# Kernel tuning notes

Hardware: AMD Instinct MI355X
Metric: run time of the kernel (lower is better)

## Reference

```python
import jax, jax.numpy as jnp
import numpy as np

B, T, D, H, L, V = 4, 1024, 1024, 16, 6, 32000
HS = D // H
FF = 4 * D
EPS = 1e-5


def setup_inputs() -> dict:
    key = jax.random.key(0)
    ks = jax.random.split(key, 16)
    s = 0.02
    n = lambda k, shape: (jax.random.normal(k, shape, jnp.float32) * s)
    return {
        'idx': jax.random.randint(ks[0], (B, T), 0, V),
        'targets': jax.random.randint(ks[1], (B, T), 0, V),
        'tok_emb': n(ks[2], (V, D)),
        'pos_emb': n(ks[3], (T, D)),
        'Wq': n(ks[4], (L, D, H, HS)),
        'Wk': n(ks[5], (L, D, H, HS)),
        'Wv': n(ks[6], (L, D, H, HS)),
        'proj_w': n(ks[7], (L, D, D)),
        'proj_b': jnp.zeros((L, D), jnp.float32),
        'ln1_g': jnp.ones((L, D), jnp.float32),
        'ln1_b': jnp.zeros((L, D), jnp.float32),
        'ln2_g': jnp.ones((L, D), jnp.float32),
        'ln2_b': jnp.zeros((L, D), jnp.float32),
        'ff_w1': n(ks[8], (L, D, FF)),
        'ff_b1': jnp.zeros((L, FF), jnp.float32),
        'ff_w2': n(ks[9], (L, FF, D)),
        'ff_b2': jnp.zeros((L, D), jnp.float32),
        'lnf_g': jnp.ones((D,), jnp.float32),
        'lnf_b': jnp.zeros((D,), jnp.float32),
        'head_w': n(ks[10], (D, V)),
        'head_b': jnp.zeros((V,), jnp.float32),
    }


def _ln(x, g, b):
    m = jnp.mean(x, axis=-1, keepdims=True)
    v = jnp.mean((x - m) ** 2, axis=-1, keepdims=True)
    return (x - m) * jax.lax.rsqrt(v + EPS) * g + b


def _forward(idx, targets, tok_emb, pos_emb, Wq, Wk, Wv, proj_w, proj_b,
             ln1_g, ln1_b, ln2_g, ln2_b, ff_w1, ff_b1, ff_w2, ff_b2,
             lnf_g, lnf_b, head_w, head_b):
    b, t = idx.shape
    x = tok_emb[idx] + pos_emb[:t]                       # [B,T,D]
    mask = jnp.tril(jnp.ones((t, t), bool))              # causal
    scale = jnp.float32(D) ** -0.5                       # NOTE: scales by num_dims (c), as in source
    for l in range(L):
        h = _ln(x, ln1_g[l], ln1_b[l])
        q = jnp.einsum('btd,dhs->bhts', h, Wq[l])        # [B,H,T,HS]
        k = jnp.einsum('btd,dhs->bhts', h, Wk[l])
        v = jnp.einsum('btd,dhs->bhts', h, Wv[l])
        w = jnp.einsum('bhts,bhus->bhtu', q, k) * scale  # [B,H,T,T]
        w = jnp.where(mask, w, -jnp.inf)
        w = jax.nn.softmax(w, axis=-1)
        o = jnp.einsum('bhtu,bhus->bhts', w, v)          # [B,H,T,HS]
        o = o.transpose(0, 2, 1, 3).reshape(b, t, D)     # concat heads
        x = x + jnp.einsum('btd,de->bte', o, proj_w[l]) + proj_b[l]
        h2 = _ln(x, ln2_g[l], ln2_b[l])
        ff = jax.nn.relu(jnp.einsum('btd,df->btf', h2, ff_w1[l]) + ff_b1[l])
        x = x + jnp.einsum('btf,fd->btd', ff, ff_w2[l]) + ff_b2[l]
    x = _ln(x, lnf_g, lnf_b)
    logits = jnp.einsum('btd,dv->btv', x, head_w) + head_b
    logits = logits.reshape(b * t, V)
    tgt = targets.reshape(b * t)
    logp = jax.nn.log_softmax(logits, axis=-1)
    loss = -jnp.mean(jnp.take_along_axis(logp, tgt[:, None], axis=-1))
    return logits, loss


def reference(idx, targets, tok_emb, pos_emb, Wq, Wk, Wv, proj_w, proj_b,
              ln1_g, ln1_b, ln2_g, ln2_b, ff_w1, ff_b1, ff_w2, ff_b2,
              lnf_g, lnf_b, head_w, head_b):
    return _forward(idx, targets, tok_emb, pos_emb, Wq, Wk, Wv, proj_w, proj_b,
                    ln1_g, ln1_b, ln2_g, ln2_b, ff_w1, ff_b1, ff_w2, ff_b2,
                    lnf_g, lnf_b, head_w, head_b)
```

## Files before the change

### kernel.cpp

```cpp
#include <hip/hip_runtime.h>

typedef __attribute__((ext_vector_type(8))) short bf16x8;
typedef __attribute__((ext_vector_type(4))) float f32x4;

#define L_LAYERS 6
#define T_SEQ 1024
#define D_MODEL 1024
#define N_HEAD 16
#define HS 64
#define FF_DIM 4096
#define VOCAB 32000
#define BT_ROWS 4096
#define ATTN_SCALE 0.03125f

__device__ __forceinline__ ushort f2bf(float f) {
  unsigned u = __builtin_bit_cast(unsigned, f);
  unsigned r = (u + 0x7fffu + ((u >> 16) & 1u)) >> 16;
  return (ushort)r;
}
__device__ __forceinline__ float waveRedSum(float v) {
#pragma unroll
  for (int off = 32; off; off >>= 1) v += __shfl_xor(v, off);
  return v;
}
__device__ __forceinline__ void gload16(const void* g, void* l) {
  __builtin_amdgcn_global_load_lds(
      (const __attribute__((address_space(1))) unsigned int*)g,
      (__attribute__((address_space(3))) unsigned int*)l, 16, 0, 0);
}

__global__ __launch_bounds__(256) void embed_kernel(const int* __restrict__ idx,
                                                    const float* __restrict__ tok,
                                                    const float* __restrict__ pos,
                                                    float* __restrict__ x) {
  int row = blockIdx.x;
  int tid = threadIdx.x;
  int t = row & (T_SEQ - 1);
  int id = idx[row];
  float4 tv = ((const float4*)(tok + (size_t)id * D_MODEL))[tid];
  float4 pv = ((const float4*)(pos + (size_t)t * D_MODEL))[tid];
  tv.x += pv.x; tv.y += pv.y; tv.z += pv.z; tv.w += pv.w;
  ((float4*)(x + (size_t)row * D_MODEL))[tid] = tv;
}

__global__ __launch_bounds__(256) void ln_kernel(const float* __restrict__ x,
                                                 const float* __restrict__ g,
                                                 const float* __restrict__ b,
                                                 ushort* __restrict__ out) {
  int row = blockIdx.x;
  int tid = threadIdx.x;
  __shared__ float red[4];
  float4 xv = ((const float4*)(x + (size_t)row * D_MODEL))[tid];
  float s = xv.x + xv.y + xv.z + xv.w;
  s = waveRedSum(s);
  if ((tid & 63) == 0) red[tid >> 6] = s;
  __syncthreads();
  float mean = (red[0] + red[1] + red[2] + red[3]) * (1.0f / D_MODEL);
  __syncthreads();
  float d0 = xv.x - mean, d1 = xv.y - mean, d2 = xv.z - mean, d3 = xv.w - mean;
  float v = d0 * d0 + d1 * d1 + d2 * d2 + d3 * d3;
  v = waveRedSum(v);
  if ((tid & 63) == 0) red[tid >> 6] = v;
  __syncthreads();
  float var = (red[0] + red[1] + red[2] + red[3]) * (1.0f / D_MODEL);
  float rstd = rsqrtf(var + 1e-5f);
  float4 gv = ((const float4*)g)[tid];
  float4 bv = ((const float4*)b)[tid];
  ushort4 o;
  o.x = f2bf(d0 * rstd * gv.x + bv.x);
  o.y = f2bf(d1 * rstd * gv.y + bv.y);
  o.z = f2bf(d2 * rstd * gv.z + bv.z);
  o.w = f2bf(d3 * rstd * gv.w + bv.w);
  ((ushort4*)(out + (size_t)row * D_MODEL))[tid] = o;
}

__device__ __forceinline__ void wconv_body(const float* __restrict__ W,
                                           ushort* __restrict__ WT,
                                           int Kd, int Nd, int n0, int k0) {
  __shared__ ushort tile[64][72];
  int tid = threadIdx.x;
#pragma unroll
  for (int i = 0; i < 4; i++) {
    int c = tid + i * 256;
    int row = c >> 4, cc = c & 15;
    float4 wv = *(const float4*)&W[(size_t)(k0 + row) * Nd + n0 + cc * 4];
    tile[row][cc * 4 + 0] = f2bf(wv.x);
    tile[row][cc * 4 + 1] = f2bf(wv.y);
    tile[row][cc * 4 + 2] = f2bf(wv.z);
    tile[row][cc * 4 + 3] = f2bf(wv.w);
  }
  __syncthreads();
#pragma unroll
  for (int i = 0; i < 2; i++) {
    int c = tid + i * 256;
    int n = c >> 3, kc = c & 7;
    __align__(16) ushort tmp[8];
#pragma unroll
    for (int j = 0; j < 8; j++) tmp[j] = tile[kc * 8 + j][n];
    *(int4*)&WT[(size_t)(n0 + n) * Kd + k0 + kc * 8] = *(const int4*)tmp;
  }
}

__global__ __launch_bounds__(256) void wconv_kernel(const float* __restrict__ W,
                                                    ushort* __restrict__ WT,
                                                    int Kd, int Nd) {
  wconv_body(W, WT, Kd, Nd, blockIdx.x * 64, blockIdx.y * 64);
}

__global__ __launch_bounds__(256) void wconv4_kernel(const float* __restrict__ W0,
                                                     const float* __restrict__ W1,
                                                     const float* __restrict__ W2,
                                                     const float* __restrict__ W3,
                                                     ushort* __restrict__ WT,
                                                     int Kd, int Nd) {
  int z = blockIdx.z;
  const float* W = (z == 0) ? W0 : (z == 1) ? W1 : (z == 2) ? W2 : W3;
  wconv_body(W, WT + (size_t)z * Kd * Nd, Kd, Nd, blockIdx.x * 64, blockIdx.y * 64);
}

__global__ __launch_bounds__(256) void vtrans_kernel(const ushort* __restrict__ v,
                                                     ushort* __restrict__ vT) {
  __shared__ ushort tile[64][72];
  int bh = blockIdx.y;
  int t0 = blockIdx.x * 64;
  int tid = threadIdx.x;
#pragma unroll
  for (int i = 0; i < 2; i++) {
    int c = tid + i * 256;
    int row = c >> 3, cc = c & 7;
    *(int4*)&tile[row][cc * 8] =
        *(const int4*)&v[((size_t)bh * T_SEQ + t0 + row) * HS + cc * 8];
  }
  __syncthreads();
#pragma unroll
  for (int i = 0; i < 2; i++) {
    int c = tid + i * 256;
    int hs = c >> 3, tc = c & 7;
    __align__(16) ushort tmp[8];
#pragma unroll
    for (int j = 0; j < 8; j++) tmp[j] = tile[tc * 8 + j][hs];
    *(int4*)&vT[((size_t)bh * HS + hs) * T_SEQ + t0 + tc * 8] = *(const int4*)tmp;
  }
}

template <int BM, int BN, int WM, int WN, int EPI>
__global__ __launch_bounds__(WM * WN * 64, 2) void gemmp_kernel(
    const ushort* __restrict__ A, const ushort* __restrict__ BT, int K,
    const float* __restrict__ bias, float* __restrict__ outf,
    ushort* __restrict__ outb, ushort* __restrict__ outk,
    ushort* __restrict__ outv, int ldo) {
  constexpr int PM = BM / WM, PN = BN / WN;
  constexpr int MR = PM / 16, NR = PN / 16;
  constexpr int ROWS = BM + BN;
  constexpr int NWAVES = WM * WN;
  constexpr int LPW = (ROWS / 8) / NWAVES;
  __shared__ __align__(16) ushort buf[2][ROWS * 64];
  int tid = threadIdx.x;
  int lane = tid & 63, wave = tid >> 6;
  int wm = wave / WN, wn = wave % WN;
  int a = lane & 15, gg = lane >> 4;
  int srow8 = lane >> 3;
  int scol8 = ((lane & 7) ^ (lane >> 3)) * 8;
  int m0 = blockIdx.y * BM, n0 = blockIdx.x * BN;
  f32x4 acc[MR][NR] = {};
  int nt = K >> 6;

  auto STAGE = [&](int t, int d) {
    int k0 = t * 64;
#pragma unroll
    for (int j = 0; j < LPW; j++) {
      int r0 = (wave * LPW + j) * 8;
      if (r0 < BM) {
        gload16(&A[(size_t)(m0 + r0 + srow8) * K + k0 + scol8], &buf[d][r0 * 64]);
      } else {
        gload16(&BT[(size_t)(n0 + (r0 - BM) + srow8) * K + k0 + scol8], &buf[d][r0 * 64]);
      }
    }
  };

  auto COMPUTE = [&](int d) {
    const ushort* bA = &buf[d][0];
    const ushort* bB = &buf[d][BM * 64];
#pragma unroll
    for (int s = 0; s < 2; s++) {
      bf16x8 af[MR], bfr[NR];
#pragma unroll
      for (int i = 0; i < MR; i++) {
        int row = wm * PM + i * 16 + a;
        af[i] = *(const bf16x8*)&bA[row * 64 + (((s * 4 + gg) ^ (a & 7)) * 8)];
      }
#pragma unroll
      for (int j = 0; j < NR; j++) {
        int row = wn * PN + j * 16 + a;
        bfr[j] = *(const bf16x8*)&bB[row * 64 + (((s * 4 + gg) ^ (a & 7)) * 8)];
      }
#pragma unroll
      for (int i = 0; i < MR; i++)
#pragma unroll
        for (int j = 0; j < NR; j++)
          acc[i][j] = __builtin_amdgcn_mfma_f32_16x16x32_bf16(af[i], bfr[j], acc[i][j], 0, 0, 0);
    }
  };

  STAGE(0, 0);
  __syncthreads();
  int cur = 0;
  for (int t = 0; t < nt; t++) {
    if (t + 1 < nt) STAGE(t + 1, cur ^ 1);
    COMPUTE(cur);
    __syncthreads();
    cur ^= 1;
  }

#pragma unroll
  for (int i = 0; i < MR; i++) {
#pragma unroll
    for (int j = 0; j < NR; j++) {
#pragma unroll
      for (int r = 0; r < 4; r++) {
        int mrow = m0 + wm * PM + i * 16 + gg * 4 + r;
        int ncol = n0 + wn * PN + j * 16 + a;
        float v = acc[i][j][r];
        if (EPI == 0) {
          int which = ncol >> 10;
          int n1 = ncol & 1023;
          int h = n1 >> 6, sidx = n1 & 63;
          int bb = mrow >> 10, tt = mrow & 1023;
          ushort* dst = (which == 0) ? outb : (which == 1) ? outk : outv;
          dst[(((size_t)(bb * N_HEAD + h)) * T_SEQ + tt) * HS + sidx] = f2bf(v);
        } else if (EPI == 1) {
          outf[(size_t)mrow * ldo + ncol] += v + bias[ncol];
        } else if (EPI == 2) {
          float t2 = v + bias[ncol];
          outb[(size_t)mrow * ldo + ncol] = f2bf(t2 > 0.0f ? t2 : 0.0f);
        } else {
          outf[(size_t)mrow * ldo + ncol] = v + bias[ncol];
        }
      }
    }
  }
}

template <int EPI, bool SWZ>
__global__ __launch_bounds__(512, 2) void gemm8_kernel(
    const ushort* __restrict__ A, const ushort* __restrict__ BT, int K,
    const float* __restrict__ bias, float* __restrict__ outf,
    ushort* __restrict__ outb, ushort* __restrict__ outk,
    ushort* __restrict__ outv, int ldo, float2* __restrict__ part) {
  extern __shared__ __align__(16) ushort lds[];
  int tid = threadIdx.x;
  int lane = tid & 63, wave = tid >> 6;
  int wm = wave >> 2, wn = wave & 3;
  int a = lane & 15, gg = lane >> 4;
  int bx = blockIdx.x, by = blockIdx.y;
  if (SWZ) {
    int gx = gridDim.x, gy = gridDim.y;
    int nwg = gx * gy;
    int wg = by * gx + bx;
    int id = (wg & 7) * (nwg >> 3) + (wg >> 3);
    by = id % gy; bx = id / gy;
  }
  int m0 = by * 256, n0 = bx * 256;
  int srow = lane >> 3;
  int scol = ((lane & 7) ^ (lane >> 3)) * 8;
  int nt = K >> 6;
  f32x4 acc[8][4] = {};

  auto stageHalf = [&](int t, int which) {
    int d = t & 1;
    int k0 = t * 64;
    const ushort* src = (which < 2) ? A : BT;
    int base0 = ((which < 2) ? m0 : n0) + (which & 1) * 128;
    ushort* dst = lds + ((which < 2) ? 0 : 32768) + d * 16384 + (which & 1) * 8192;
#pragma unroll
    for (int q = 0; q < 2; q++) {
      int r0 = q * 64 + wave * 8;
      gload16(&src[(size_t)(base0 + r0 + srow) * K + k0 + scol], dst + r0 * 64);
    }
  };

  stageHalf(0, 0); stageHalf(0, 1); stageHalf(0, 2); stageHalf(0, 3);
  if (nt > 1) {
    stageHalf(1, 2); stageHalf(1, 3);
    asm volatile("s_waitcnt vmcnt(4)" ::: "memory");
  } else {
    asm volatile("s_waitcnt vmcnt(0)" ::: "memory");
  }
  __builtin_amdgcn_sched_barrier(0);
  __builtin_amdgcn_s_barrier();

  for (int t = 0; t < nt; t++) {
    int d = t & 1;
    const ushort* bA = lds + d * 16384;
    const ushort* bB = lds + 32768 + d * 16384;
    bf16x8 alo[4][2], ahi[4][2], bj01[2][2], bj23[2][2];
#pragma unroll
    for (int i = 0; i < 4; i++)
#pragma unroll
      for (int s = 0; s < 2; s++) {
        int row = wm * 128 + i * 16 + a;
        alo[i][s] = *(const bf16x8*)&bA[row * 64 + (((s * 4 + gg) ^ (a & 7)) * 8)];
      }
#pragma unroll
    for (int j = 0; j < 2; j++)
#pragma unroll
      for (int s = 0; s < 2; s++) {
        int row = wn * 64 + j * 16 + a;
        bj01[j][s] = *(const bf16x8*)&bB[row * 64 + (((s * 4 + gg) ^ (a & 7)) * 8)];
      }
    if (t + 1 < nt) stageHalf(t + 1, 0);
    __builtin_amdgcn_s_barrier();
    asm volatile("s_waitcnt lgkmcnt(0)" ::: "memory");
    __builtin_amdgcn_sched_barrier(0);
    __builtin_amdgcn_s_setprio(1);
#pragma unroll
    for (int i = 0; i < 4; i++)
#pragma unroll
      for (int j = 0; j < 2; j++)
#pragma unroll
        for (int s = 0; s < 2; s++)
          acc[i][j] = __builtin_amdgcn_mfma_f32_16x16x32_bf16(alo[i][s], bj01[j][s], acc[i][j], 0, 0, 0);
    __builtin_amdgcn_s_setprio(0);
    __builtin_amdgcn_s_barrier();
#pragma unroll
    for (int j = 0; j < 2; j++)
#pragma unroll
      for (int s = 0; s < 2; s++) {
        int row = wn * 64 + (j + 2) * 16 + a;
        bj23[j][s] = *(const bf16x8*)&bB[row * 64 + (((s * 4 + gg) ^ (a & 7)) * 8)];
      }
    if (t + 1 < nt) stageHalf(t + 1, 1);
    __builtin_amdgcn_s_barrier();
    asm volatile("s_waitcnt lgkmcnt(0)" ::: "memory");
    __builtin_amdgcn_sched_barrier(0);
    __builtin_amdgcn_s_setprio(1);
#pragma unroll
    for (int i = 0; i < 4; i++)
#pragma unroll
      for (int j = 0; j < 2; j++)
#pragma unroll
        for (int s = 0; s < 2; s++)
          acc[i][j + 2] = __builtin_amdgcn_mfma_f32_16x16x32_bf16(alo[i][s], bj23[j][s], acc[i][j + 2], 0, 0, 0);
    __builtin_amdgcn_s_setprio(0);
    __builtin_amdgcn_s_barrier();
#pragma unroll
    for (int i = 0; i < 4; i++)
#pragma unroll
      for (int s = 0; s < 2; s++) {
        int row = wm * 128 + (i + 4) * 16 + a;
        ahi[i][s] = *(const bf16x8*)&bA[row * 64 + (((s * 4 + gg) ^ (a & 7)) * 8)];
      }
    if (t + 2 < nt) stageHalf(t + 2, 2);
    __builtin_amdgcn_s_barrier();
    asm volatile("s_waitcnt lgkmcnt(0)" ::: "memory");
    __builtin_amdgcn_sched_barrier(0);
    __builtin_amdgcn_s_setprio(1);
#pragma unroll
    for (int i = 0; i < 4; i++)
#pragma unroll
      for (int j = 0; j < 2; j++)
#pragma unroll
        for (int s = 0; s < 2; s++)
          acc[i + 4][j] = __builtin_amdgcn_mfma_f32_16x16x32_bf16(ahi[i][s], bj01[j][s], acc[i + 4][j], 0, 0, 0);
    __builtin_amdgcn_s_setprio(0);
    __builtin_amdgcn_s_barrier();
    if (t + 2 < nt) stageHalf(t + 2, 3);
    __builtin_amdgcn_s_barrier();
    __builtin_amdgcn_s_setprio(1);
#pragma unroll
    for (int i = 0; i < 4; i++)
#pragma unroll
      for (int j = 0; j < 2; j++)
#pragma unroll
        for (int s = 0; s < 2; s++)
          acc[i + 4][j + 2] = __builtin_amdgcn_mfma_f32_16x16x32_bf16(ahi[i][s], bj23[j][s], acc[i + 4][j + 2], 0, 0, 0);
    __builtin_amdgcn_s_setprio(0);
    __builtin_amdgcn_sched_barrier(0);
    if (t + 1 < nt) {
      if (t + 2 < nt) asm volatile("s_waitcnt vmcnt(4)" ::: "memory");
      else            asm volatile("s_waitcnt vmcnt(0)" ::: "memory");
      __builtin_amdgcn_sched_barrier(0);
    }
    __builtin_amdgcn_s_barrier();
  }

  if (EPI == 3) {
    float bj[4];
#pragma unroll
    for (int j = 0; j < 4; j++) bj[j] = bias[n0 + wn * 64 + j * 16 + a];
#pragma unroll
    for (int i = 0; i < 8; i++)
#pragma unroll
      for (int j = 0; j < 4; j++)
#pragma unroll
        for (int r = 0; r < 4; r++) acc[i][j][r] += bj[j];
#pragma unroll
    for (int i = 0; i < 8; i++)
#pragma unroll
      for (int j = 0; j < 4; j++)
#pragma unroll
        for (int r = 0; r < 4; r++) {
          int mrow = m0 + wm * 128 + i * 16 + gg * 4 + r;
          int ncol = n0 + wn * 64 + j * 16 + a;
          outf[(size_t)mrow * ldo + ncol] = acc[i][j][r];
        }
    float2* sm = (float2*)lds;
#pragma unroll
    for (int i = 0; i < 8; i++) {
#pragma unroll
      for (int r = 0; r < 4; r++) {
        float pm = fmaxf(fmaxf(acc[i][0][r], acc[i][1][r]),
                         fmaxf(acc[i][2][r], acc[i][3][r]));
#pragma unroll
        for (int off = 1; off < 16; off <<= 1) pm = fmaxf(pm, __shfl_xor(pm, off));
        float ps = __expf(acc[i][0][r] - pm) + __expf(acc[i][1][r] - pm) +
                   __expf(acc[i][2][r] - pm) + __expf(acc[i][3][r] - pm);
#pragma unroll
        for (int off = 1; off < 16; off <<= 1) ps += __shfl_xor(ps, off);
        if (a == 0) {
          float2 v2; v2.x = pm; v2.y = ps;
          sm[(wm * 128 + i * 16 + gg * 4 + r) * 4 + wn] = v2;
        }
      }
    }
    __syncthreads();
    if (tid < 256) {
      float2 p0 = sm[tid * 4 + 0], p1 = sm[tid * 4 + 1];
      float2 p2 = sm[tid * 4 + 2], p3 = sm[tid * 4 + 3];
      float M = fmaxf(fmaxf(p0.x, p1.x), fmaxf(p2.x, p3.x));
      float S = p0.y * __expf(p0.x - M) + p1.y * __expf(p1.x - M) +
                p2.y * __expf(p2.x - M) + p3.y * __expf(p3.x - M);
      float2 o2; o2.x = M; o2.y = S;
      part[(size_t)(m0 + tid) * 128 + (n0 >> 8)] = o2;
    }
    return;
  }

#pragma unroll
  for (int i = 0; i < 8; i++) {
#pragma unroll
    for (int j = 0; j < 4; j++) {
#pragma unroll
      for (int r = 0; r < 4; r++) {
        int mrow = m0 + wm * 128 + i * 16 + gg * 4 + r;
        int ncol = n0 + wn * 64 + j * 16 + a;
        float v = acc[i][j][r];
        if (EPI == 0) {
          int which = ncol >> 10;
          int n1 = ncol & 1023;
          int h = n1 >> 6, sidx = n1 & 63;
          int bb = mrow >> 10, tt = mrow & 1023;
          ushort* dst = (which == 0) ? outb : (which == 1) ? outk : outv;
          dst[(((size_t)(bb * N_HEAD + h)) * T_SEQ + tt) * HS + sidx] = f2bf(v);
        } else if (EPI == 2) {
          float t2 = v + bias[ncol];
          outb[(size_t)mrow * ldo + ncol] = f2bf(t2 > 0.0f ? t2 : 0.0f);
        }
      }
    }
  }
}

__global__ __launch_bounds__(256) void attn_kernel(const ushort* __restrict__ q,
                                                   const ushort* __restrict__ k,
                                                   const ushort* __restrict__ vT,
                                                   ushort* __restrict__ o) {
  __shared__ __align__(16) ushort Psm[4][16 * 72];
  int tid = threadIdx.x;
  int lane = tid & 63, w = tid >> 6;
  int a = lane & 15, gg = lane >> 4;
  int qt = blockIdx.x, bh = blockIdx.y;
  int qrow_b = qt * 64 + w * 16;
  int qmy = qrow_b + a;

  bf16x8 qf[2];
  const ushort* qbase = q + ((size_t)bh * T_SEQ + qmy) * HS;
  qf[0] = *(const bf16x8*)&qbase[gg * 8];
  qf[1] = *(const bf16x8*)&qbase[32 + gg * 8];

  const ushort* kbase = k + (size_t)bh * T_SEQ * HS;
  const ushort* vbase = vT + (size_t)bh * HS * T_SEQ;

  float m_run = -__builtin_inff();
  float l_run = 0.0f;
  f32x4 oacc[4] = {};
  int nkt = qt + 1;

  for (int kt = 0; kt < nkt; kt++) {
    int k0 = kt * 64;

    f32x4 st[4] = {};
    __builtin_amdgcn_s_setprio(1);
#pragma unroll
    for (int ku = 0; ku < 4; ku++) {
#pragma unroll
      for (int s = 0; s < 2; s++) {
        bf16x8 kf = *(const bf16x8*)&kbase[(size_t)(k0 + ku * 16 + a) * HS + s * 32 + gg * 8];
        st[ku] = __builtin_amdgcn_mfma_f32_16x16x32_bf16(kf, qf[s], st[ku], 0, 0, 0);
      }
    }
    __builtin_amdgcn_s_setprio(0);

    float pv[16];
    float pm = -__builtin_inff();
#pragma unroll
    for (int ku = 0; ku < 4; ku++) {
#pragma unroll
      for (int r = 0; r < 4; r++) {
        int u = k0 + ku * 16 + gg * 4 + r;
        float val = (u <= qmy) ? st[ku][r] * ATTN_SCALE : -__builtin_inff();
        pv[ku * 4 + r] = val;
        pm = fmaxf(pm, val);
      }
    }
    pm = fmaxf(pm, __shfl_xor(pm, 16));
    pm = fmaxf(pm, __shfl_xor(pm, 32));
    float m_new = fmaxf(m_run, pm);
    float cfac = __expf(m_run - m_new);
    float tsum = 0.0f;
#pragma unroll
    for (int xi = 0; xi < 16; xi++) {
      float p = __expf(pv[xi] - m_new);
      pv[xi] = p;
      tsum += p;
    }
    tsum += __shfl_xor(tsum, 16);
    tsum += __shfl_xor(tsum, 32);
    l_run = l_run * cfac + tsum;
    m_run = m_new;

    ushort* P = (ushort*)&Psm[w][0];
    asm volatile("s_waitcnt lgkmcnt(0)" ::: "memory");
#pragma unroll
    for (int ku = 0; ku < 4; ku++) {
      ushort4 pw;
      pw.x = f2bf(pv[ku * 4 + 0]);
      pw.y = f2bf(pv[ku * 4 + 1]);
      pw.z = f2bf(pv[ku * 4 + 2]);
      pw.w = f2bf(pv[ku * 4 + 3]);
      *(ushort4*)&P[a * 72 + ku * 16 + gg * 4] = pw;
    }
#pragma unroll
    for (int r = 0; r < 4; r++) {
      float cr = __shfl(cfac, gg * 4 + r);
#pragma unroll
      for (int nb = 0; nb < 4; nb++) oacc[nb][r] *= cr;
    }
    asm volatile("s_waitcnt lgkmcnt(0)" ::: "memory");
    __builtin_amdgcn_s_setprio(1);
#pragma unroll
    for (int kb = 0; kb < 2; kb++) {
      bf16x8 pa = *(const bf16x8*)&P[a * 72 + kb * 32 + gg * 8];
#pragma unroll
      for (int nb = 0; nb < 4; nb++) {
        bf16x8 vb = *(const bf16x8*)&vbase[(size_t)(nb * 16 + a) * T_SEQ + k0 + kb * 32 + gg * 8];
        oacc[nb] = __builtin_amdgcn_mfma_f32_16x16x32_bf16(pa, vb, oacc[nb], 0, 0, 0);
      }
    }
    __builtin_amdgcn_s_setprio(0);
  }

  float linv = 1.0f / l_run;
  int bb = bh >> 4, hh = bh & 15;
#pragma unroll
  for (int r = 0; r < 4; r++) {
    float li = __shfl(linv, gg * 4 + r);
    int qr = qrow_b + gg * 4 + r;
#pragma unroll
    for (int nb = 0; nb < 4; nb++) {
      o[((size_t)(bb * T_SEQ + qr)) * D_MODEL + hh * HS + nb * 16 + a] =
          f2bf(oacc[nb][r] * li);
    }
  }
}

__global__ __launch_bounds__(64) void loss_rows_kernel(const float2* __restrict__ part,
                                                       const float* __restrict__ logits,
                                                       const int* __restrict__ tgt,
                                                       float* __restrict__ row_loss) {
  int row = blockIdx.x;
  int l = threadIdx.x;
  float m = -__builtin_inff(), s = 0.0f;
#pragma unroll
  for (int q = 0; q < 2; q++) {
    int c = l * 2 + q;
    if (c < 125) {
      float2 p = part[(size_t)row * 128 + c];
      float nm = fmaxf(m, p.x);
      s = s * __expf(m - nm) + p.y * __expf(p.x - nm);
      m = nm;
    }
  }
#pragma unroll
  for (int off = 1; off < 64; off <<= 1) {
    float om = __shfl_xor(m, off), os = __shfl_xor(s, off);
    float nm = fmaxf(m, om);
    s = s * __expf(m - nm) + os * __expf(om - nm);
    m = nm;
  }
  if (l == 0)
    row_loss[row] = m + logf(s) - logits[(size_t)row * VOCAB + tgt[row]];
}

__global__ __launch_bounds__(256) void loss_final_kernel(const float* __restrict__ row_loss,
                                                         float* __restrict__ out) {
  int tid = threadIdx.x;
  __shared__ float red[4];
  float s = 0.0f;
  for (int i = tid; i < BT_ROWS; i += 256) s += row_loss[i];
  s = waveRedSum(s);
  if ((tid & 63) == 0) red[tid >> 6] = s;
  __syncthreads();
  if (tid == 0) out[0] = (red[0] + red[1] + red[2] + red[3]) * (1.0f / BT_ROWS);
}

extern "C" void kernel_launch(void* const* d_in, const int* in_sizes, int n_in,
                              void* d_out, int out_size, void* d_ws, size_t ws_size,
                              hipStream_t stream) {
  const int* idx = (const int*)d_in[0];
  const int* tgt = (const int*)d_in[1];
  const float* tok_emb = (const float*)d_in[2];
  const float* pos_emb = (const float*)d_in[3];
  const float* Wq = (const float*)d_in[4];
  const float* Wk = (const float*)d_in[5];
  const float* Wv = (const float*)d_in[6];
  const float* proj_w = (const float*)d_in[7];
  const float* proj_b = (const float*)d_in[8];
  const float* ln1_g = (const float*)d_in[9];
  const float* ln1_b = (const float*)d_in[10];
  const float* ln2_g = (const float*)d_in[11];
  const float* ln2_b = (const float*)d_in[12];
  const float* ff_w1 = (const float*)d_in[13];
  const float* ff_b1 = (const float*)d_in[14];
  const float* ff_w2 = (const float*)d_in[15];
  const float* ff_b2 = (const float*)d_in[16];
  const float* lnf_g = (const float*)d_in[17];
  const float* lnf_b = (const float*)d_in[18];
  const float* head_w = (const float*)d_in[19];
  const float* head_b = (const float*)d_in[20];

  char* ws = (char*)d_ws;
  size_t off = 0;
  float* x = (float*)(ws + off); off += (size_t)BT_ROWS * D_MODEL * 4;
  ushort* h = (ushort*)(ws + off); off += (size_t)BT_ROWS * D_MODEL * 2;
  ushort* qb = (ushort*)(ws + off); off += (size_t)BT_ROWS * D_MODEL * 2;
  ushort* kb = (ushort*)(ws + off); off += (size_t)BT_ROWS * D_MODEL * 2;
  ushort* vb = (ushort*)(ws + off); off += (size_t)BT_ROWS * D_MODEL * 2;
  ushort* vTb = (ushort*)(ws + off); off += (size_t)BT_ROWS * D_MODEL * 2;
  ushort* ob = (ushort*)(ws + off); off += (size_t)BT_ROWS * D_MODEL * 2;
  ushort* ffb = (ushort*)(ws + off); off += (size_t)BT_ROWS * FF_DIM * 2;
  ushort* wqkvT = (ushort*)(ws + off); off += (size_t)4 * D_MODEL * D_MODEL * 2;
  ushort* wprojT = wqkvT + (size_t)3 * D_MODEL * D_MODEL;
  ushort* wff1T = (ushort*)(ws + off); off += (size_t)FF_DIM * D_MODEL * 2;
  ushort* wff2T = (ushort*)(ws + off); off += (size_t)D_MODEL * FF_DIM * 2;
  float* row_loss = (float*)(ws + off); off += (size_t)BT_ROWS * 4;
  float2* part = (float2*)(ws + off); off += (size_t)BT_ROWS * 128 * 8;
  ushort* headT = qb;

  float* logits = (float*)d_out;

  embed_kernel<<<BT_ROWS, 256, 0, stream>>>(idx, tok_emb, pos_emb, x);

  for (int l = 0; l < L_LAYERS; l++) {
    size_t wo = (size_t)l * D_MODEL * D_MODEL;
    size_t fo = (size_t)l * D_MODEL * FF_DIM;
    wconv4_kernel<<<dim3(16, 16, 4), 256, 0, stream>>>(Wq + wo, Wk + wo, Wv + wo, proj_w + wo,
                                                       wqkvT, D_MODEL, D_MODEL);
    wconv_kernel<<<dim3(64, 16), 256, 0, stream>>>(ff_w1 + fo, wff1T, D_MODEL, FF_DIM);
    wconv_kernel<<<dim3(16, 64), 256, 0, stream>>>(ff_w2 + fo, wff2T, FF_DIM, D_MODEL);

    ln_kernel<<<BT_ROWS, 256, 0, stream>>>(x, ln1_g + l * D_MODEL, ln1_b + l * D_MODEL, h);
    gemm8_kernel<0, false><<<dim3(12, 16), 512, 131072, stream>>>(
        h, wqkvT, D_MODEL, nullptr, nullptr, qb, kb, vb, 0, nullptr);
    vtrans_kernel<<<dim3(16, 64), 256, 0, stream>>>(vb, vTb);
    attn_kernel<<<dim3(16, 64), 256, 0, stream>>>(qb, kb, vTb, ob);
    gemmp_kernel<64, 128, 2, 2, 1><<<dim3(8, 64), 256, 0, stream>>>(
        ob, wprojT, D_MODEL, proj_b + l * D_MODEL, x, nullptr, nullptr, nullptr, D_MODEL);
    ln_kernel<<<BT_ROWS, 256, 0, stream>>>(x, ln2_g + l * D_MODEL, ln2_b + l * D_MODEL, h);
    gemm8_kernel<2, false><<<dim3(16, 16), 512, 131072, stream>>>(
        h, wff1T, D_MODEL, ff_b1 + (size_t)l * FF_DIM, nullptr, ffb, nullptr, nullptr,
        FF_DIM, nullptr);
    gemmp_kernel<64, 128, 2, 2, 1><<<dim3(8, 64), 256, 0, stream>>>(
        ffb, wff2T, FF_DIM, ff_b2 + l * D_MODEL, x, nullptr, nullptr, nullptr, D_MODEL);
  }

  ln_kernel<<<BT_ROWS, 256, 0, stream>>>(x, lnf_g, lnf_b, h);

  wconv_kernel<<<dim3(500, 16), 256, 0, stream>>>(head_w, headT, D_MODEL, VOCAB);
  gemm8_kernel<3, true><<<dim3(125, 16), 512, 131072, stream>>>(
      h, headT, D_MODEL, head_b, logits, nullptr, nullptr, nullptr, VOCAB, part);

  loss_rows_kernel<<<BT_ROWS, 64, 0, stream>>>(part, logits, tgt, row_loss);
  loss_final_kernel<<<1, 256, 0, stream>>>(row_loss, logits + (size_t)BT_ROWS * VOCAB);
}
```

Before: 2.227 ms.

## Stage attention K/V in LDS, use wave-per-row layernorm, enlarge residual GEMM tiles

Attention now double-buffers each 64-key K and V tile in shared memory through registers, so MFMA operands come from LDS rather than strided global loads, at the cost of a block barrier per key tile. LayerNorm assigns one wave per row with four rows per block, which removes the shared-memory reductions and block barriers. The projection and FFN2 GEMMs move from 64-row to 128-row tiles, halving the grid. The swizzled head-GEMM block remap is changed to decompose the id along x instead of y.

```diff
diff --git a/kernel.cpp b/kernel.cpp
--- a/kernel.cpp
+++ b/kernel.cpp
@@ -47,31 +47,40 @@
                                                  const float* __restrict__ g,
                                                  const float* __restrict__ b,
                                                  ushort* __restrict__ out) {
-  int row = blockIdx.x;
   int tid = threadIdx.x;
-  __shared__ float red[4];
-  float4 xv = ((const float4*)(x + (size_t)row * D_MODEL))[tid];
-  float s = xv.x + xv.y + xv.z + xv.w;
+  int lane = tid & 63, w = tid >> 6;
+  int row = blockIdx.x * 4 + w;
+  const float4* xr = (const float4*)(x + (size_t)row * D_MODEL);
+  float4 xv[4];
+#pragma unroll
+  for (int i = 0; i < 4; i++) xv[i] = xr[lane + i * 64];
+  float s = 0.0f;
+#pragma unroll
+  for (int i = 0; i < 4; i++) s += xv[i].x + xv[i].y + xv[i].z + xv[i].w;
   s = waveRedSum(s);
-  if ((tid & 63) == 0) red[tid >> 6] = s;
-  __syncthreads();
-  float mean = (red[0] + red[1] + red[2] + red[3]) * (1.0f / D_MODEL);
-  __syncthreads();
-  float d0 = xv.x - mean, d1 = xv.y - mean, d2 = xv.z - mean, d3 = xv.w - mean;
-  float v = d0 * d0 + d1 * d1 + d2 * d2 + d3 * d3;
+  float mean = s * (1.0f / D_MODEL);
+  float v = 0.0f;
+#pragma unroll
+  for (int i = 0; i < 4; i++) {
+    float d0 = xv[i].x - mean, d1 = xv[i].y - mean;
+    float d2 = xv[i].z - mean, d3 = xv[i].w - mean;
+    v += d0 * d0 + d1 * d1 + d2 * d2 + d3 * d3;
+  }
   v = waveRedSum(v);
-  if ((tid & 63) == 0) red[tid >> 6] = v;
-  __syncthreads();
-  float var = (red[0] + red[1] + red[2] + red[3]) * (1.0f / D_MODEL);
-  float rstd = rsqrtf(var + 1e-5f);
-  float4 gv = ((const float4*)g)[tid];
-  float4 bv = ((const float4*)b)[tid];
-  ushort4 o;
-  o.x = f2bf(d0 * rstd * gv.x + bv.x);
-  o.y = f2bf(d1 * rstd * gv.y + bv.y);
-  o.z = f2bf(d2 * rstd * gv.z + bv.z);
-  o.w = f2bf(d3 * rstd * gv.w + bv.w);
-  ((ushort4*)(out + (size_t)row * D_MODEL))[tid] = o;
+  float rstd = rsqrtf(v * (1.0f / D_MODEL) + 1e-5f);
+  const float4* gr = (const float4*)g;
+  const float4* br = (const float4*)b;
+  ushort4* orow = (ushort4*)(out + (size_t)row * D_MODEL);
+#pragma unroll
+  for (int i = 0; i < 4; i++) {
+    float4 gv = gr[lane + i * 64], bv = br[lane + i * 64];
+    ushort4 o;
+    o.x = f2bf((xv[i].x - mean) * rstd * gv.x + bv.x);
+    o.y = f2bf((xv[i].y - mean) * rstd * gv.y + bv.y);
+    o.z = f2bf((xv[i].z - mean) * rstd * gv.z + bv.z);
+    o.w = f2bf((xv[i].w - mean) * rstd * gv.w + bv.w);
+    orow[lane + i * 64] = o;
+  }
 }
 
 __device__ __forceinline__ void wconv_body(const float* __restrict__ W,
@@ -258,7 +267,7 @@
     int nwg = gx * gy;
     int wg = by * gx + bx;
     int id = (wg & 7) * (nwg >> 3) + (wg >> 3);
-    by = id % gy; bx = id / gy;
+    bx = id % gx; by = id / gx;
   }
   int m0 = by * 256, n0 = bx * 256;
   int srow = lane >> 3;
@@ -465,6 +474,8 @@
                                                    const ushort* __restrict__ k,
                                                    const ushort* __restrict__ vT,
                                                    ushort* __restrict__ o) {
+  __shared__ __align__(16) ushort Ksm[2][64 * 72];
+  __shared__ __align__(16) ushort Vsm[2][64 * 72];
   __shared__ __align__(16) ushort Psm[4][16 * 72];
   int tid = threadIdx.x;
   int lane = tid & 63, w = tid >> 6;
@@ -478,16 +489,48 @@
   qf[0] = *(const bf16x8*)&qbase[gg * 8];
   qf[1] = *(const bf16x8*)&qbase[32 + gg * 8];
 
-  const ushort* kbase = k + (size_t)bh * T_SEQ * HS;
-  const ushort* vbase = vT + (size_t)bh * HS * T_SEQ;
+  const ushort* kbp = k + (size_t)bh * T_SEQ * HS;
+  const ushort* vbp = vT + (size_t)bh * HS * T_SEQ;
+
+  int c0 = tid, c1 = tid + 256;
+  int row0 = c0 >> 3, cc0 = c0 & 7;
+  int row1 = c1 >> 3, cc1 = c1 & 7;
+
+  auto LOADR = [&](int kt, int4& k0r, int4& k1r, int4& v0r, int4& v1r) {
+    int k0 = kt * 64;
+    k0r = *(const int4*)&kbp[(size_t)(k0 + row0) * HS + cc0 * 8];
+    k1r = *(const int4*)&kbp[(size_t)(k0 + row1) * HS + cc1 * 8];
+    v0r = *(const int4*)&vbp[(size_t)row0 * T_SEQ + k0 + cc0 * 8];
+    v1r = *(const int4*)&vbp[(size_t)row1 * T_SEQ + k0 + cc1 * 8];
+  };
+  auto WRITEL = [&](int d, const int4& k0r, const int4& k1r,
+                    const int4& v0r, const int4& v1r) {
+    *(int4*)&Ksm[d][row0 * 72 + cc0 * 8] = k0r;
+    *(int4*)&Ksm[d][row1 * 72 + cc1 * 8] = k1r;
+    *(int4*)&Vsm[d][row0 * 72 + cc0 * 8] = v0r;
+    *(int4*)&Vsm[d][row1 * 72 + cc1 * 8] = v1r;
+  };
 
   float m_run = -__builtin_inff();
   float l_run = 0.0f;
   f32x4 oacc[4] = {};
   int nkt = qt + 1;
 
+  {
+    int4 ka, kb2, va, vb2;
+    LOADR(0, ka, kb2, va, vb2);
+    WRITEL(0, ka, kb2, va, vb2);
+  }
+  __syncthreads();
+  int cur = 0;
+
   for (int kt = 0; kt < nkt; kt++) {
     int k0 = kt * 64;
+    int4 nka, nkb, nva, nvb;
+    if (kt + 1 < nkt) LOADR(kt + 1, nka, nkb, nva, nvb);
+
+    const ushort* Ks = Ksm[cur];
+    const ushort* Vs = Vsm[cur];
 
     f32x4 st[4] = {};
     __builtin_amdgcn_s_setprio(1);
@@ -495,7 +538,7 @@
     for (int ku = 0; ku < 4; ku++) {
 #pragma unroll
       for (int s = 0; s < 2; s++) {
-        bf16x8 kf = *(const bf16x8*)&kbase[(size_t)(k0 + ku * 16 + a) * HS + s * 32 + gg * 8];
+        bf16x8 kf = *(const bf16x8*)&Ks[(ku * 16 + a) * 72 + s * 32 + gg * 8];
         st[ku] = __builtin_amdgcn_mfma_f32_16x16x32_bf16(kf, qf[s], st[ku], 0, 0, 0);
       }
     }
@@ -549,15 +592,19 @@
     asm volatile("s_waitcnt lgkmcnt(0)" ::: "memory");
     __builtin_amdgcn_s_setprio(1);
 #pragma unroll
-    for (int kb = 0; kb < 2; kb++) {
-      bf16x8 pa = *(const bf16x8*)&P[a * 72 + kb * 32 + gg * 8];
+    for (int kb2 = 0; kb2 < 2; kb2++) {
+      bf16x8 pa = *(const bf16x8*)&P[a * 72 + kb2 * 32 + gg * 8];
 #pragma unroll
       for (int nb = 0; nb < 4; nb++) {
-        bf16x8 vb = *(const bf16x8*)&vbase[(size_t)(nb * 16 + a) * T_SEQ + k0 + kb * 32 + gg * 8];
-        oacc[nb] = __builtin_amdgcn_mfma_f32_16x16x32_bf16(pa, vb, oacc[nb], 0, 0, 0);
+        bf16x8 vb2 = *(const bf16x8*)&Vs[(nb * 16 + a) * 72 + kb2 * 32 + gg * 8];
+        oacc[nb] = __builtin_amdgcn_mfma_f32_16x16x32_bf16(pa, vb2, oacc[nb], 0, 0, 0);
       }
     }
     __builtin_amdgcn_s_setprio(0);
+
+    if (kt + 1 < nkt) WRITEL(cur ^ 1, nka, nkb, nva, nvb);
+    __syncthreads();
+    cur ^= 1;
   }
 
   float linv = 1.0f / l_run;
@@ -669,22 +716,22 @@
     wconv_kernel<<<dim3(64, 16), 256, 0, stream>>>(ff_w1 + fo, wff1T, D_MODEL, FF_DIM);
     wconv_kernel<<<dim3(16, 64), 256, 0, stream>>>(ff_w2 + fo, wff2T, FF_DIM, D_MODEL);
 
-    ln_kernel<<<BT_ROWS, 256, 0, stream>>>(x, ln1_g + l * D_MODEL, ln1_b + l * D_MODEL, h);
+    ln_kernel<<<BT_ROWS / 4, 256, 0, stream>>>(x, ln1_g + l * D_MODEL, ln1_b + l * D_MODEL, h);
     gemm8_kernel<0, false><<<dim3(12, 16), 512, 131072, stream>>>(
         h, wqkvT, D_MODEL, nullptr, nullptr, qb, kb, vb, 0, nullptr);
     vtrans_kernel<<<dim3(16, 64), 256, 0, stream>>>(vb, vTb);
     attn_kernel<<<dim3(16, 64), 256, 0, stream>>>(qb, kb, vTb, ob);
-    gemmp_kernel<64, 128, 2, 2, 1><<<dim3(8, 64), 256, 0, stream>>>(
+    gemmp_kernel<128, 128, 2, 2, 1><<<dim3(8, 32), 256, 0, stream>>>(
         ob, wprojT, D_MODEL, proj_b + l * D_MODEL, x, nullptr, nullptr, nullptr, D_MODEL);
-    ln_kernel<<<BT_ROWS, 256, 0, stream>>>(x, ln2_g + l * D_MODEL, ln2_b + l * D_MODEL, h);
+    ln_kernel<<<BT_ROWS / 4, 256, 0, stream>>>(x, ln2_g + l * D_MODEL, ln2_b + l * D_MODEL, h);
     gemm8_kernel<2, false><<<dim3(16, 16), 512, 131072, stream>>>(
         h, wff1T, D_MODEL, ff_b1 + (size_t)l * FF_DIM, nullptr, ffb, nullptr, nullptr,
         FF_DIM, nullptr);
-    gemmp_kernel<64, 128, 2, 2, 1><<<dim3(8, 64), 256, 0, stream>>>(
+    gemmp_kernel<128, 128, 2, 2, 1><<<dim3(8, 32), 256, 0, stream>>>(
         ffb, wff2T, FF_DIM, ff_b2 + l * D_MODEL, x, nullptr, nullptr, nullptr, D_MODEL);
   }
 
-  ln_kernel<<<BT_ROWS, 256, 0, stream>>>(x, lnf_g, lnf_b, h);
+  ln_kernel<<<BT_ROWS / 4, 256, 0, stream>>>(x, lnf_g, lnf_b, h);
 
   wconv_kernel<<<dim3(500, 16), 256, 0, stream>>>(head_w, headT, D_MODEL, VOCAB);
   gemm8_kernel<3, true><<<dim3(125, 16), 512, 131072, stream>>>(
```

After: 1.933 ms. 1.15x faster.
